# Performance work log

Measured on AMD Instinct MI355X. Metric: run time of the kernel, lower is better.

## Reference

```python
import jax, jax.numpy as jnp
import numpy as np


def setup_inputs() -> dict:
    key = jax.random.key(0)
    ks = jax.random.split(key, 9)
    B, C, H, W = 16, 64, 64, 64
    s = 0.02
    return {
        "x": jax.random.normal(ks[0], (B, C, H, W), dtype=jnp.float32),
        "qw": jax.random.normal(ks[1], (C, C), dtype=jnp.float32) * s,
        "qb": jax.random.normal(ks[2], (C,), dtype=jnp.float32) * s,
        "kw": jax.random.normal(ks[3], (C, C), dtype=jnp.float32) * s,
        "kb": jax.random.normal(ks[4], (C,), dtype=jnp.float32) * s,
        "vw": jax.random.normal(ks[5], (C, C), dtype=jnp.float32) * s,
        "vb": jax.random.normal(ks[6], (C,), dtype=jnp.float32) * s,
        "ow": jax.random.normal(ks[7], (C, C), dtype=jnp.float32) * s,
        "ob": jax.random.normal(ks[8], (C,), dtype=jnp.float32) * s,
    }


def reference(x, qw, qb, kw, kb, vw, vb, ow, ob):
    # x: [B, C, H, W]; 1x1 convs == per-pixel linear maps with weight [out_ch, in_ch]
    B, C, H, W = x.shape
    S = H * W
    xt = x.reshape(B, C, S).transpose(0, 2, 1)  # [B, S, C] tokens over spatial positions
    Q = jnp.einsum("bsc,oc->bso", xt, qw) + qb
    K = jnp.einsum("bsc,oc->bso", xt, kw) + kb
    V = jnp.einsum("bsc,oc->bso", xt, vw) + vb
    scale = 1.0 / jnp.sqrt(jnp.asarray(C, dtype=x.dtype))
    scores = jnp.einsum("bqc,bkc->bqk", Q, K) * scale  # [B, S, S]
    attn = jax.nn.softmax(scores, axis=-1)
    out = jnp.einsum("bqk,bkc->bqc", attn, V)  # [B, S, C]
    out = jnp.einsum("bsc,oc->bso", out, ow) + ob  # out 1x1 conv
    return out.transpose(0, 2, 1).reshape(B, C, H, W)
```

## Files before the change

### kernel.cpp

```cpp
#include <hip/hip_runtime.h>
#include <stdint.h>

#define SS 4096
#define CC 64
#define BB 16

typedef unsigned short u16;
typedef __attribute__((ext_vector_type(8))) __bf16 bf16x8;
typedef __attribute__((ext_vector_type(8))) short short8;
typedef __attribute__((ext_vector_type(4))) float f32x4;

__device__ __forceinline__ uint32_t pkbf(float a, float b) {
    uint32_t ua = __float_as_uint(a) + 0x8000u;
    uint32_t ub = __float_as_uint(b) + 0x8000u;
    return __builtin_amdgcn_perm(ub, ua, 0x07060302u);
}

__global__ void wpre_kernel(const float* __restrict__ qw, const float* __restrict__ kw,
                            const float* __restrict__ vw, const float* __restrict__ ow,
                            u16* __restrict__ wsb)
{
    int idx = blockIdx.x * 256 + threadIdx.x;
    const float* src = (idx < 2048) ? qw : (idx < 4096) ? kw
                     : (idx < 6144) ? vw : ow;
    int pair = idx & 2047;
    ((uint32_t*)wsb)[idx] = pkbf(src[pair * 2], src[pair * 2 + 1]);
}

__global__ __launch_bounds__(256, 4) void qkv_kernel(
    const float* __restrict__ x, const u16* __restrict__ wsb,
    const float* __restrict__ qb, const float* __restrict__ kb,
    const float* __restrict__ vb,
    u16* __restrict__ Q, u16* __restrict__ K, u16* __restrict__ VT)
{
    const int b    = blockIdx.x & 15;
    const int s0   = (blockIdx.x >> 4) << 6;
    const int tid  = threadIdx.x;
    const int w    = tid >> 6;
    const int lane = tid & 63;
    const int lq   = lane & 15;
    const int quad = lane >> 4;

    __shared__ u16 xt[64 * 72];
    __shared__ u16 bounce[4][16 * 72];

    {
        const int sl = tid & 63;
        const int g  = tid >> 6;
        const float* xp = x + (size_t)b * CC * SS + s0 + sl;
#pragma unroll
        for (int i = 0; i < 8; ++i) {
            int p = g + (i << 2);
            float f0 = xp[(size_t)(2 * p) * SS];
            float f1 = xp[(size_t)(2 * p + 1) * SS];
            ((uint32_t*)&xt[sl * 72])[p] = pkbf(f0, f1);
        }
    }
    __syncthreads();

    bf16x8 a0 = *(const bf16x8*)&xt[(w * 16 + lq) * 72 + quad * 8];
    bf16x8 a1 = *(const bf16x8*)&xt[(w * 16 + lq) * 72 + 32 + quad * 8];

    const float QSCALE = 0.125f * 1.44269504088896340736f;

    for (int m = 0; m < 3; ++m) {
        const float* bsrc = (m == 0) ? qb : ((m == 1) ? kb : vb);
        const u16* wm = wsb + m * 4096;
        bf16x8 bfr[2][4];
#pragma unroll
        for (int kc = 0; kc < 2; ++kc)
#pragma unroll
            for (int nt = 0; nt < 4; ++nt)
                bfr[kc][nt] = *(const bf16x8*)&wm[(nt * 16 + lq) * 64 + kc * 32 + quad * 8];

        f32x4 acc[4];
#pragma unroll
        for (int nt = 0; nt < 4; ++nt) {
            float bv = bsrc[nt * 16 + lq];
            acc[nt] = (f32x4){bv, bv, bv, bv};
        }
#pragma unroll
        for (int nt = 0; nt < 4; ++nt) {
            acc[nt] = __builtin_amdgcn_mfma_f32_16x16x32_bf16(a0, bfr[0][nt], acc[nt], 0, 0, 0);
            acc[nt] = __builtin_amdgcn_mfma_f32_16x16x32_bf16(a1, bfr[1][nt], acc[nt], 0, 0, 0);
        }

        if (m == 2) {
#pragma unroll
            for (int nt = 0; nt < 4; ++nt) {
                int c = nt * 16 + lq;
                uint2 pv;
                pv.x = pkbf(acc[nt][0], acc[nt][1]);
                pv.y = pkbf(acc[nt][2], acc[nt][3]);
                *(uint2*)(VT + ((size_t)(b * CC + c)) * SS + s0 + w * 16 + quad * 4) = pv;
            }
        } else {
            const float scl = (m == 0) ? QSCALE : 1.0f;
            u16* bb = bounce[w];
#pragma unroll
            for (int nt = 0; nt < 4; ++nt)
#pragma unroll
                for (int r = 0; r < 4; ++r)
                    bb[(quad * 4 + r) * 72 + nt * 16 + lq] =
                        (u16)((__float_as_uint(acc[nt][r] * scl) + 0x8000u) >> 16);

            const int row = lane >> 2;
            const int ch  = (lane & 3) << 4;
            short8 v0 = *(const short8*)&bb[row * 72 + ch];
            short8 v1 = *(const short8*)&bb[row * 72 + ch + 8];
            u16* dst = ((m == 0) ? Q : K) + ((size_t)(b * SS + s0 + w * 16 + row)) * CC + ch;
            *(short8*)dst = v0;
            *(short8*)(dst + 8) = v1;
        }
    }
}

__global__ __launch_bounds__(256, 2) void flash_kernel(
    const u16* __restrict__ Q, const u16* __restrict__ K,
    const u16* __restrict__ Vt, const u16* __restrict__ owb,
    const float* __restrict__ ob, float* __restrict__ out)
{
    const int b    = blockIdx.x & 15;
    const int q0   = (blockIdx.x >> 4) << 7;
    const int tid  = threadIdx.x;
    const int w    = tid >> 6;
    const int lane = tid & 63;
    const int lq   = lane & 15;
    const int quad = lane >> 4;

    __shared__ u16 lds_k[2][64 * 64];
    __shared__ u16 lds_v[2][64 * 64];
    __shared__ u16 lds_p[8][16 * 72];

    bf16x8 qf[2][2];
#pragma unroll
    for (int g = 0; g < 2; ++g) {
        const u16* qp = Q + ((size_t)(b * SS + q0 + g * 64 + w * 16 + lq)) * CC + quad * 8;
        qf[g][0] = *(const bf16x8*)(qp);
        qf[g][1] = *(const bf16x8*)(qp + 32);
    }

    f32x4 ot[2][4];
#pragma unroll
    for (int g = 0; g < 2; ++g)
#pragma unroll
        for (int ct = 0; ct < 4; ++ct) ot[g][ct] = (f32x4){0.f, 0.f, 0.f, 0.f};
    float lp[2][4] = {{0.f, 0.f, 0.f, 0.f}, {0.f, 0.f, 0.f, 0.f}};

    const int srow = tid >> 2;
    const int a    = tid & 3;
    const u16* kg = K + ((size_t)(b * SS + srow)) * CC + a * 16;
    const u16* vg = Vt + ((size_t)(b * CC + srow)) * SS + a * 16;
    const int sw0 = srow * 64 + (((a << 1)    ) ^ (srow & 7)) * 8;
    const int sw1 = srow * 64 + (((a << 1) | 1) ^ (srow & 7)) * 8;

    {
        short8 k0 = *(const short8*)(kg);
        short8 k1 = *(const short8*)(kg + 8);
        short8 v0 = *(const short8*)(vg);
        short8 v1 = *(const short8*)(vg + 8);
        *(short8*)&lds_k[0][sw0] = k0;
        *(short8*)&lds_k[0][sw1] = k1;
        *(short8*)&lds_v[0][sw0] = v0;
        *(short8*)&lds_v[0][sw1] = v1;
    }

    const int lsw = lq & 7;
    u16* pw0 = lds_p[(w << 1)];
    u16* pw1 = lds_p[(w << 1) | 1];

    for (int kt = 0; kt < 64; ++kt) {
        __syncthreads();
        const int buf = kt & 1;

        const int ktn = (kt + 1) & 63;
        const u16* kgn = kg + (size_t)ktn * (64 * CC);
        const u16* vgn = vg + ktn * 64;
        short8 nk0 = *(const short8*)(kgn);
        short8 nk1 = *(const short8*)(kgn + 8);
        short8 nv0 = *(const short8*)(vgn);
        short8 nv1 = *(const short8*)(vgn + 8);

        bf16x8 kf[2][4];
#pragma unroll
        for (int kc = 0; kc < 2; ++kc)
#pragma unroll
            for (int mt = 0; mt < 4; ++mt)
                kf[kc][mt] = *(const bf16x8*)
                    &lds_k[buf][(mt * 16 + lq) * 64 + (((kc << 2) + quad) ^ lsw) * 8];

        f32x4 sa[2][4];
#pragma unroll
        for (int g = 0; g < 2; ++g)
#pragma unroll
            for (int mt = 0; mt < 4; ++mt) sa[g][mt] = (f32x4){0.f, 0.f, 0.f, 0.f};
#pragma unroll
        for (int g = 0; g < 2; ++g)
#pragma unroll
            for (int kc = 0; kc < 2; ++kc)
#pragma unroll
                for (int mt = 0; mt < 4; ++mt)
                    sa[g][mt] = __builtin_amdgcn_mfma_f32_16x16x32_bf16(
                        kf[kc][mt], qf[g][kc], sa[g][mt], 0, 0, 0);

#pragma unroll
        for (int g = 0; g < 2; ++g) {
            u16* pw = g ? pw1 : pw0;
#pragma unroll
            for (int mt = 0; mt < 4; ++mt) {
                float p0 = __builtin_amdgcn_exp2f(sa[g][mt][0]);
                float p1 = __builtin_amdgcn_exp2f(sa[g][mt][1]);
                float p2 = __builtin_amdgcn_exp2f(sa[g][mt][2]);
                float p3 = __builtin_amdgcn_exp2f(sa[g][mt][3]);
                lp[g][0] += p0; lp[g][1] += p1; lp[g][2] += p2; lp[g][3] += p3;
                uint2 pv;
                pv.x = pkbf(p0, p1);
                pv.y = pkbf(p2, p3);
                *(uint2*)&pw[lq * 72 + mt * 16 + quad * 4] = pv;
            }
        }

        bf16x8 vf[2][4];
#pragma unroll
        for (int kc = 0; kc < 2; ++kc)
#pragma unroll
            for (int ct = 0; ct < 4; ++ct)
                vf[kc][ct] = *(const bf16x8*)
                    &lds_v[buf][(ct * 16 + lq) * 64 + (((kc << 2) + quad) ^ lsw) * 8];

#pragma unroll
        for (int g = 0; g < 2; ++g) {
            const u16* pw = g ? pw1 : pw0;
#pragma unroll
            for (int kc = 0; kc < 2; ++kc) {
                bf16x8 pf = *(const bf16x8*)&pw[lq * 72 + kc * 32 + quad * 8];
#pragma unroll
                for (int ct = 0; ct < 4; ++ct)
                    ot[g][ct] = __builtin_amdgcn_mfma_f32_16x16x32_bf16(
                        vf[kc][ct], pf, ot[g][ct], 0, 0, 0);
            }
        }

        u16* lkd = lds_k[buf ^ 1];
        u16* lvd = lds_v[buf ^ 1];
        *(short8*)&lkd[sw0] = nk0;
        *(short8*)&lkd[sw1] = nk1;
        *(short8*)&lvd[sw0] = nv0;
        *(short8*)&lvd[sw1] = nv1;
    }

    bf16x8 wf[2][4];
#pragma unroll
    for (int kc = 0; kc < 2; ++kc)
#pragma unroll
        for (int nt = 0; nt < 4; ++nt)
            wf[kc][nt] = *(const bf16x8*)&owb[(nt * 16 + lq) * 64 + kc * 32 + quad * 8];
    float bias[4];
#pragma unroll
    for (int nt = 0; nt < 4; ++nt) bias[nt] = ob[nt * 16 + lq];

#pragma unroll
    for (int g = 0; g < 2; ++g) {
        float l = (lp[g][0] + lp[g][1]) + (lp[g][2] + lp[g][3]);
        l += __shfl_xor(l, 16);
        l += __shfl_xor(l, 32);
        const float inv = 1.0f / l;

        u16* po = g ? pw1 : pw0;
#pragma unroll
        for (int ct = 0; ct < 4; ++ct) {
            uint2 pv;
            pv.x = pkbf(ot[g][ct][0] * inv, ot[g][ct][1] * inv);
            pv.y = pkbf(ot[g][ct][2] * inv, ot[g][ct][3] * inv);
            *(uint2*)&po[lq * 72 + ct * 16 + quad * 4] = pv;
        }
        bf16x8 oa0 = *(const bf16x8*)&po[lq * 72 + quad * 8];
        bf16x8 oa1 = *(const bf16x8*)&po[lq * 72 + 32 + quad * 8];

        f32x4 acc[4];
#pragma unroll
        for (int nt = 0; nt < 4; ++nt)
            acc[nt] = (f32x4){bias[nt], bias[nt], bias[nt], bias[nt]};
#pragma unroll
        for (int nt = 0; nt < 4; ++nt) {
            acc[nt] = __builtin_amdgcn_mfma_f32_16x16x32_bf16(oa0, wf[0][nt], acc[nt], 0, 0, 0);
            acc[nt] = __builtin_amdgcn_mfma_f32_16x16x32_bf16(oa1, wf[1][nt], acc[nt], 0, 0, 0);
        }
#pragma unroll
        for (int nt = 0; nt < 4; ++nt) {
            float* dst = out + ((size_t)(b * CC + nt * 16 + lq)) * SS
                       + q0 + g * 64 + w * 16 + quad * 4;
            *(f32x4*)dst = acc[nt];
        }
    }
}

extern "C" void kernel_launch(void* const* d_in, const int* in_sizes, int n_in,
                              void* d_out, int out_size, void* d_ws, size_t ws_size,
                              hipStream_t stream)
{
    const float* x  = (const float*)d_in[0];
    const float* qw = (const float*)d_in[1];
    const float* qb = (const float*)d_in[2];
    const float* kw = (const float*)d_in[3];
    const float* kb = (const float*)d_in[4];
    const float* vw = (const float*)d_in[5];
    const float* vb = (const float*)d_in[6];
    const float* ow = (const float*)d_in[7];
    const float* ob = (const float*)d_in[8];
    float* out = (float*)d_out;

    const size_t T = (size_t)BB * SS * CC;
    u16* WSB = (u16*)d_ws;
    u16* Q   = WSB + 4 * 4096;
    u16* K   = Q + T;
    u16* VT  = K + T;

    wpre_kernel<<<dim3(32), dim3(256), 0, stream>>>(qw, kw, vw, ow, WSB);
    qkv_kernel<<<dim3(BB * 64), dim3(256), 0, stream>>>(x, WSB, qb, kb, vb, Q, K, VT);
    flash_kernel<<<dim3(BB * 32), dim3(256), 0, stream>>>(Q, K, VT, WSB + 3 * 4096, ob, out);
}
```

Before: 188.9 us.

## Split flash kernel key tiles across waves and load QKV inputs directly to registers

The flash kernel now splits each 64-key tile between wave pairs. Each wave covers 64 queries but only 32 keys, so it loads half the K fragments and a reduced V fragment set from LDS per query group. The two key-halves' partial outputs and row sums are then merged through LDS before the output projection, which only half the waves perform. The QKV kernel drops its LDS transpose of x and reads the strided fp32 values straight into MFMA operand registers. This cuts LDS traffic per MFMA, at the cost of more accumulator registers, a final cross-wave reduction, and less-coalesced global reads of x.

```diff
diff --git a/kernel.cpp b/kernel.cpp
--- a/kernel.cpp
+++ b/kernel.cpp
@@ -41,25 +41,23 @@
     const int lq   = lane & 15;
     const int quad = lane >> 4;
 
-    __shared__ u16 xt[64 * 72];
     __shared__ u16 bounce[4][16 * 72];
 
-    {
-        const int sl = tid & 63;
-        const int g  = tid >> 6;
-        const float* xp = x + (size_t)b * CC * SS + s0 + sl;
-#pragma unroll
-        for (int i = 0; i < 8; ++i) {
-            int p = g + (i << 2);
-            float f0 = xp[(size_t)(2 * p) * SS];
-            float f1 = xp[(size_t)(2 * p + 1) * SS];
-            ((uint32_t*)&xt[sl * 72])[p] = pkbf(f0, f1);
-        }
-    }
-    __syncthreads();
-
-    bf16x8 a0 = *(const bf16x8*)&xt[(w * 16 + lq) * 72 + quad * 8];
-    bf16x8 a1 = *(const bf16x8*)&xt[(w * 16 + lq) * 72 + 32 + quad * 8];
+    const int sm = s0 + w * 16 + lq;
+    const float* xp = x + (size_t)b * CC * SS + sm;
+    float xf[16];
+#pragma unroll
+    for (int kc = 0; kc < 2; ++kc)
+#pragma unroll
+        for (int j = 0; j < 8; ++j)
+            xf[kc * 8 + j] = xp[(size_t)(kc * 32 + quad * 8 + j) * SS];
+
+    union { uint32_t u[4]; bf16x8 v; } A0, A1;
+#pragma unroll
+    for (int p = 0; p < 4; ++p) {
+        A0.u[p] = pkbf(xf[2 * p],     xf[2 * p + 1]);
+        A1.u[p] = pkbf(xf[8 + 2 * p], xf[8 + 2 * p + 1]);
+    }
 
     const float QSCALE = 0.125f * 1.44269504088896340736f;
 
@@ -81,8 +79,8 @@
         }
 #pragma unroll
         for (int nt = 0; nt < 4; ++nt) {
-            acc[nt] = __builtin_amdgcn_mfma_f32_16x16x32_bf16(a0, bfr[0][nt], acc[nt], 0, 0, 0);
-            acc[nt] = __builtin_amdgcn_mfma_f32_16x16x32_bf16(a1, bfr[1][nt], acc[nt], 0, 0, 0);
+            acc[nt] = __builtin_amdgcn_mfma_f32_16x16x32_bf16(A0.v, bfr[0][nt], acc[nt], 0, 0, 0);
+            acc[nt] = __builtin_amdgcn_mfma_f32_16x16x32_bf16(A1.v, bfr[1][nt], acc[nt], 0, 0, 0);
         }
 
         if (m == 2) {
@@ -124,28 +122,29 @@
     const int q0   = (blockIdx.x >> 4) << 7;
     const int tid  = threadIdx.x;
     const int w    = tid >> 6;
+    const int qh   = w & 1;
+    const int kh   = w >> 1;
     const int lane = tid & 63;
     const int lq   = lane & 15;
     const int quad = lane >> 4;
 
-    __shared__ u16 lds_k[2][64 * 64];
-    __shared__ u16 lds_v[2][64 * 64];
-    __shared__ u16 lds_p[8][16 * 72];
-
-    bf16x8 qf[2][2];
-#pragma unroll
-    for (int g = 0; g < 2; ++g) {
-        const u16* qp = Q + ((size_t)(b * SS + q0 + g * 64 + w * 16 + lq)) * CC + quad * 8;
+    __shared__ u16 lds_s[2][8192];
+    __shared__ u16 lds_p[4][2048];
+
+    bf16x8 qf[4][2];
+#pragma unroll
+    for (int g = 0; g < 4; ++g) {
+        const u16* qp = Q + ((size_t)(b * SS + q0 + qh * 64 + g * 16 + lq)) * CC + quad * 8;
         qf[g][0] = *(const bf16x8*)(qp);
         qf[g][1] = *(const bf16x8*)(qp + 32);
     }
 
-    f32x4 ot[2][4];
-#pragma unroll
-    for (int g = 0; g < 2; ++g)
+    f32x4 ot[4][4];
+#pragma unroll
+    for (int g = 0; g < 4; ++g)
 #pragma unroll
         for (int ct = 0; ct < 4; ++ct) ot[g][ct] = (f32x4){0.f, 0.f, 0.f, 0.f};
-    float lp[2][4] = {{0.f, 0.f, 0.f, 0.f}, {0.f, 0.f, 0.f, 0.f}};
+    float lp[4] = {0.f, 0.f, 0.f, 0.f};
 
     const int srow = tid >> 2;
     const int a    = tid & 3;
@@ -159,15 +158,15 @@
         short8 k1 = *(const short8*)(kg + 8);
         short8 v0 = *(const short8*)(vg);
         short8 v1 = *(const short8*)(vg + 8);
-        *(short8*)&lds_k[0][sw0] = k0;
-        *(short8*)&lds_k[0][sw1] = k1;
-        *(short8*)&lds_v[0][sw0] = v0;
-        *(short8*)&lds_v[0][sw1] = v1;
+        *(short8*)&lds_s[0][sw0] = k0;
+        *(short8*)&lds_s[0][sw1] = k1;
+        *(short8*)&lds_s[0][4096 + sw0] = v0;
+        *(short8*)&lds_s[0][4096 + sw1] = v1;
     }
 
     const int lsw = lq & 7;
-    u16* pw0 = lds_p[(w << 1)];
-    u16* pw1 = lds_p[(w << 1) | 1];
+    u16* pw = lds_p[w];
+    const int ps = lq & 1;
 
     for (int kt = 0; kt < 64; ++kt) {
         __syncthreads();
@@ -181,116 +180,128 @@
         short8 nv0 = *(const short8*)(vgn);
         short8 nv1 = *(const short8*)(vgn + 8);
 
-        bf16x8 kf[2][4];
+        bf16x8 kf[2][2];
 #pragma unroll
         for (int kc = 0; kc < 2; ++kc)
 #pragma unroll
-            for (int mt = 0; mt < 4; ++mt)
+            for (int mt = 0; mt < 2; ++mt)
                 kf[kc][mt] = *(const bf16x8*)
-                    &lds_k[buf][(mt * 16 + lq) * 64 + (((kc << 2) + quad) ^ lsw) * 8];
-
-        f32x4 sa[2][4];
-#pragma unroll
-        for (int g = 0; g < 2; ++g)
-#pragma unroll
-            for (int mt = 0; mt < 4; ++mt) sa[g][mt] = (f32x4){0.f, 0.f, 0.f, 0.f};
-#pragma unroll
-        for (int g = 0; g < 2; ++g)
+                    &lds_s[buf][(kh * 32 + mt * 16 + lq) * 64 + (((kc << 2) + quad) ^ lsw) * 8];
+
+        bf16x8 vf[4];
+#pragma unroll
+        for (int ct = 0; ct < 4; ++ct)
+            vf[ct] = *(const bf16x8*)
+                &lds_s[buf][4096 + (ct * 16 + lq) * 64 + (((kh << 2) + quad) ^ lsw) * 8];
+
+#pragma unroll
+        for (int g = 0; g < 4; ++g) {
+            f32x4 sa[2];
+            sa[0] = (f32x4){0.f, 0.f, 0.f, 0.f};
+            sa[1] = (f32x4){0.f, 0.f, 0.f, 0.f};
 #pragma unroll
             for (int kc = 0; kc < 2; ++kc)
 #pragma unroll
-                for (int mt = 0; mt < 4; ++mt)
-                    sa[g][mt] = __builtin_amdgcn_mfma_f32_16x16x32_bf16(
-                        kf[kc][mt], qf[g][kc], sa[g][mt], 0, 0, 0);
-
-#pragma unroll
-        for (int g = 0; g < 2; ++g) {
-            u16* pw = g ? pw1 : pw0;
-#pragma unroll
-            for (int mt = 0; mt < 4; ++mt) {
-                float p0 = __builtin_amdgcn_exp2f(sa[g][mt][0]);
-                float p1 = __builtin_amdgcn_exp2f(sa[g][mt][1]);
-                float p2 = __builtin_amdgcn_exp2f(sa[g][mt][2]);
-                float p3 = __builtin_amdgcn_exp2f(sa[g][mt][3]);
-                lp[g][0] += p0; lp[g][1] += p1; lp[g][2] += p2; lp[g][3] += p3;
+                for (int mt = 0; mt < 2; ++mt)
+                    sa[mt] = __builtin_amdgcn_mfma_f32_16x16x32_bf16(
+                        kf[kc][mt], qf[g][kc], sa[mt], 0, 0, 0);
+
+            const int pr = (g * 16 + lq) * 32;
+#pragma unroll
+            for (int mt = 0; mt < 2; ++mt) {
+                float p0 = __builtin_amdgcn_exp2f(sa[mt][0]);
+                float p1 = __builtin_amdgcn_exp2f(sa[mt][1]);
+                float p2 = __builtin_amdgcn_exp2f(sa[mt][2]);
+                float p3 = __builtin_amdgcn_exp2f(sa[mt][3]);
+                lp[g] += (p0 + p1) + (p2 + p3);
                 uint2 pv;
                 pv.x = pkbf(p0, p1);
                 pv.y = pkbf(p2, p3);
-                *(uint2*)&pw[lq * 72 + mt * 16 + quad * 4] = pv;
-            }
-        }
-
-        bf16x8 vf[2][4];
+                *(uint2*)&pw[pr + ((mt ^ ps) << 4) + quad * 4] = pv;
+            }
+        }
+
+#pragma unroll
+        for (int g = 0; g < 4; ++g) {
+            const int pr = (g * 16 + lq) * 32;
+            bf16x8 pf = *(const bf16x8*)&pw[pr + (((quad >> 1) ^ ps) << 4) + (quad & 1) * 8];
+#pragma unroll
+            for (int ct = 0; ct < 4; ++ct)
+                ot[g][ct] = __builtin_amdgcn_mfma_f32_16x16x32_bf16(
+                    vf[ct], pf, ot[g][ct], 0, 0, 0);
+        }
+
+        u16* ld = lds_s[buf ^ 1];
+        *(short8*)&ld[sw0] = nk0;
+        *(short8*)&ld[sw1] = nk1;
+        *(short8*)&ld[4096 + sw0] = nv0;
+        *(short8*)&ld[4096 + sw1] = nv1;
+    }
+
+#pragma unroll
+    for (int g = 0; g < 4; ++g) {
+        lp[g] += __shfl_xor(lp[g], 16);
+        lp[g] += __shfl_xor(lp[g], 32);
+    }
+
+    float* mb  = (float*)&lds_s[0][0];
+    float* lpb = (float*)&lds_p[2][0];
+
+    __syncthreads();
+    if (kh == 1) {
+#pragma unroll
+        for (int g = 0; g < 4; ++g) {
+#pragma unroll
+            for (int ct = 0; ct < 4; ++ct)
+                *(f32x4*)&mb[qh * 4096 + (g * 16 + lq) * 64 + ct * 16 + quad * 4] = ot[g][ct];
+            if (quad == 0) lpb[qh * 64 + g * 16 + lq] = lp[g];
+        }
+    }
+    __syncthreads();
+
+    if (kh == 0) {
+        bf16x8 wf[2][4];
 #pragma unroll
         for (int kc = 0; kc < 2; ++kc)
 #pragma unroll
-            for (int ct = 0; ct < 4; ++ct)
-                vf[kc][ct] = *(const bf16x8*)
-                    &lds_v[buf][(ct * 16 + lq) * 64 + (((kc << 2) + quad) ^ lsw) * 8];
-
-#pragma unroll
-        for (int g = 0; g < 2; ++g) {
-            const u16* pw = g ? pw1 : pw0;
-#pragma unroll
-            for (int kc = 0; kc < 2; ++kc) {
-                bf16x8 pf = *(const bf16x8*)&pw[lq * 72 + kc * 32 + quad * 8];
-#pragma unroll
-                for (int ct = 0; ct < 4; ++ct)
-                    ot[g][ct] = __builtin_amdgcn_mfma_f32_16x16x32_bf16(
-                        vf[kc][ct], pf, ot[g][ct], 0, 0, 0);
-            }
-        }
-
-        u16* lkd = lds_k[buf ^ 1];
-        u16* lvd = lds_v[buf ^ 1];
-        *(short8*)&lkd[sw0] = nk0;
-        *(short8*)&lkd[sw1] = nk1;
-        *(short8*)&lvd[sw0] = nv0;
-        *(short8*)&lvd[sw1] = nv1;
-    }
-
-    bf16x8 wf[2][4];
-#pragma unroll
-    for (int kc = 0; kc < 2; ++kc)
-#pragma unroll
-        for (int nt = 0; nt < 4; ++nt)
-            wf[kc][nt] = *(const bf16x8*)&owb[(nt * 16 + lq) * 64 + kc * 32 + quad * 8];
-    float bias[4];
-#pragma unroll
-    for (int nt = 0; nt < 4; ++nt) bias[nt] = ob[nt * 16 + lq];
-
-#pragma unroll
-    for (int g = 0; g < 2; ++g) {
-        float l = (lp[g][0] + lp[g][1]) + (lp[g][2] + lp[g][3]);
-        l += __shfl_xor(l, 16);
-        l += __shfl_xor(l, 32);
-        const float inv = 1.0f / l;
-
-        u16* po = g ? pw1 : pw0;
-#pragma unroll
-        for (int ct = 0; ct < 4; ++ct) {
-            uint2 pv;
-            pv.x = pkbf(ot[g][ct][0] * inv, ot[g][ct][1] * inv);
-            pv.y = pkbf(ot[g][ct][2] * inv, ot[g][ct][3] * inv);
-            *(uint2*)&po[lq * 72 + ct * 16 + quad * 4] = pv;
-        }
-        bf16x8 oa0 = *(const bf16x8*)&po[lq * 72 + quad * 8];
-        bf16x8 oa1 = *(const bf16x8*)&po[lq * 72 + 32 + quad * 8];
-
-        f32x4 acc[4];
-#pragma unroll
-        for (int nt = 0; nt < 4; ++nt)
-            acc[nt] = (f32x4){bias[nt], bias[nt], bias[nt], bias[nt]};
-#pragma unroll
-        for (int nt = 0; nt < 4; ++nt) {
-            acc[nt] = __builtin_amdgcn_mfma_f32_16x16x32_bf16(oa0, wf[0][nt], acc[nt], 0, 0, 0);
-            acc[nt] = __builtin_amdgcn_mfma_f32_16x16x32_bf16(oa1, wf[1][nt], acc[nt], 0, 0, 0);
-        }
-#pragma unroll
-        for (int nt = 0; nt < 4; ++nt) {
-            float* dst = out + ((size_t)(b * CC + nt * 16 + lq)) * SS
-                       + q0 + g * 64 + w * 16 + quad * 4;
-            *(f32x4*)dst = acc[nt];
+            for (int nt = 0; nt < 4; ++nt)
+                wf[kc][nt] = *(const bf16x8*)&owb[(nt * 16 + lq) * 64 + kc * 32 + quad * 8];
+        float bias[4];
+#pragma unroll
+        for (int nt = 0; nt < 4; ++nt) bias[nt] = ob[nt * 16 + lq];
+
+        u16* po = lds_p[w];
+#pragma unroll
+        for (int g = 0; g < 4; ++g) {
+            const float l = lp[g] + lpb[qh * 64 + g * 16 + lq];
+            const float inv = 1.0f / l;
+
+#pragma unroll
+            for (int ct = 0; ct < 4; ++ct) {
+                f32x4 o2 = *(const f32x4*)&mb[qh * 4096 + (g * 16 + lq) * 64 + ct * 16 + quad * 4];
+                uint2 pv;
+                pv.x = pkbf((ot[g][ct][0] + o2[0]) * inv, (ot[g][ct][1] + o2[1]) * inv);
+                pv.y = pkbf((ot[g][ct][2] + o2[2]) * inv, (ot[g][ct][3] + o2[3]) * inv);
+                *(uint2*)&po[lq * 72 + ct * 16 + quad * 4] = pv;
+            }
+            bf16x8 oa0 = *(const bf16x8*)&po[lq * 72 + quad * 8];
+            bf16x8 oa1 = *(const bf16x8*)&po[lq * 72 + 32 + quad * 8];
+
+            f32x4 acc[4];
+#pragma unroll
+            for (int nt = 0; nt < 4; ++nt)
+                acc[nt] = (f32x4){bias[nt], bias[nt], bias[nt], bias[nt]};
+#pragma unroll
+            for (int nt = 0; nt < 4; ++nt) {
+                acc[nt] = __builtin_amdgcn_mfma_f32_16x16x32_bf16(oa0, wf[0][nt], acc[nt], 0, 0, 0);
+                acc[nt] = __builtin_amdgcn_mfma_f32_16x16x32_bf16(oa1, wf[1][nt], acc[nt], 0, 0, 0);
+            }
+#pragma unroll
+            for (int nt = 0; nt < 4; ++nt) {
+                float* dst = out + ((size_t)(b * CC + nt * 16 + lq)) * SS
+                           + q0 + qh * 64 + g * 16 + quad * 4;
+                *(f32x4*)dst = acc[nt];
+            }
         }
     }
 }
```

Result: slower. 216.5 us (+14.6%).

## Load V fragments directly from global and drop LDS staging for x and V

Applied to the files above, without the earlier changes.

In the flash kernel, V^T tiles are no longer staged through double-buffered LDS. Each lane now loads its MFMA operand fragments straight from global memory at the top of every key tile. In the QKV kernel, x is read per lane into registers and packed to bf16 without the shared transpose buffer or its barrier. This trims LDS footprint and traffic, which may allow more blocks per CU. The cost is global loads on the critical path of each iteration with no prefetch ahead of use, plus strided, less coalesced x reads.

```diff
diff --git a/kernel.cpp b/kernel.cpp
--- a/kernel.cpp
+++ b/kernel.cpp
@@ -41,25 +41,23 @@
     const int lq   = lane & 15;
     const int quad = lane >> 4;
 
-    __shared__ u16 xt[64 * 72];
     __shared__ u16 bounce[4][16 * 72];
 
-    {
-        const int sl = tid & 63;
-        const int g  = tid >> 6;
-        const float* xp = x + (size_t)b * CC * SS + s0 + sl;
-#pragma unroll
-        for (int i = 0; i < 8; ++i) {
-            int p = g + (i << 2);
-            float f0 = xp[(size_t)(2 * p) * SS];
-            float f1 = xp[(size_t)(2 * p + 1) * SS];
-            ((uint32_t*)&xt[sl * 72])[p] = pkbf(f0, f1);
-        }
-    }
-    __syncthreads();
-
-    bf16x8 a0 = *(const bf16x8*)&xt[(w * 16 + lq) * 72 + quad * 8];
-    bf16x8 a1 = *(const bf16x8*)&xt[(w * 16 + lq) * 72 + 32 + quad * 8];
+    const int sm = s0 + w * 16 + lq;
+    const float* xp = x + (size_t)b * CC * SS + sm;
+    float xf[16];
+#pragma unroll
+    for (int kc = 0; kc < 2; ++kc)
+#pragma unroll
+        for (int j = 0; j < 8; ++j)
+            xf[kc * 8 + j] = xp[(size_t)(kc * 32 + quad * 8 + j) * SS];
+
+    union { uint32_t u[4]; bf16x8 v; } A0, A1;
+#pragma unroll
+    for (int p = 0; p < 4; ++p) {
+        A0.u[p] = pkbf(xf[2 * p],     xf[2 * p + 1]);
+        A1.u[p] = pkbf(xf[8 + 2 * p], xf[8 + 2 * p + 1]);
+    }
 
     const float QSCALE = 0.125f * 1.44269504088896340736f;
 
@@ -81,8 +79,8 @@
         }
 #pragma unroll
         for (int nt = 0; nt < 4; ++nt) {
-            acc[nt] = __builtin_amdgcn_mfma_f32_16x16x32_bf16(a0, bfr[0][nt], acc[nt], 0, 0, 0);
-            acc[nt] = __builtin_amdgcn_mfma_f32_16x16x32_bf16(a1, bfr[1][nt], acc[nt], 0, 0, 0);
+            acc[nt] = __builtin_amdgcn_mfma_f32_16x16x32_bf16(A0.v, bfr[0][nt], acc[nt], 0, 0, 0);
+            acc[nt] = __builtin_amdgcn_mfma_f32_16x16x32_bf16(A1.v, bfr[1][nt], acc[nt], 0, 0, 0);
         }
 
         if (m == 2) {
@@ -129,7 +127,6 @@
     const int quad = lane >> 4;
 
     __shared__ u16 lds_k[2][64 * 64];
-    __shared__ u16 lds_v[2][64 * 64];
     __shared__ u16 lds_p[8][16 * 72];
 
     bf16x8 qf[2][2];
@@ -140,6 +137,11 @@
         qf[g][1] = *(const bf16x8*)(qp + 32);
     }
 
+    const u16* vp[4];
+#pragma unroll
+    for (int ct = 0; ct < 4; ++ct)
+        vp[ct] = Vt + ((size_t)(b * CC + ct * 16 + lq)) * SS + quad * 8;
+
     f32x4 ot[2][4];
 #pragma unroll
     for (int g = 0; g < 2; ++g)
@@ -150,19 +152,14 @@
     const int srow = tid >> 2;
     const int a    = tid & 3;
     const u16* kg = K + ((size_t)(b * SS + srow)) * CC + a * 16;
-    const u16* vg = Vt + ((size_t)(b * CC + srow)) * SS + a * 16;
     const int sw0 = srow * 64 + (((a << 1)    ) ^ (srow & 7)) * 8;
     const int sw1 = srow * 64 + (((a << 1) | 1) ^ (srow & 7)) * 8;
 
     {
         short8 k0 = *(const short8*)(kg);
         short8 k1 = *(const short8*)(kg + 8);
-        short8 v0 = *(const short8*)(vg);
-        short8 v1 = *(const short8*)(vg + 8);
         *(short8*)&lds_k[0][sw0] = k0;
         *(short8*)&lds_k[0][sw1] = k1;
-        *(short8*)&lds_v[0][sw0] = v0;
-        *(short8*)&lds_v[0][sw1] = v1;
     }
 
     const int lsw = lq & 7;
@@ -173,13 +170,17 @@
         __syncthreads();
         const int buf = kt & 1;
 
+        bf16x8 vfr[2][4];
+#pragma unroll
+        for (int kc = 0; kc < 2; ++kc)
+#pragma unroll
+            for (int ct = 0; ct < 4; ++ct)
+                vfr[kc][ct] = *(const bf16x8*)(vp[ct] + kc * 32);
+
         const int ktn = (kt + 1) & 63;
         const u16* kgn = kg + (size_t)ktn * (64 * CC);
-        const u16* vgn = vg + ktn * 64;
         short8 nk0 = *(const short8*)(kgn);
         short8 nk1 = *(const short8*)(kgn + 8);
-        short8 nv0 = *(const short8*)(vgn);
-        short8 nv1 = *(const short8*)(vgn + 8);
 
         bf16x8 kf[2][4];
 #pragma unroll
@@ -220,14 +221,6 @@
             }
         }
 
-        bf16x8 vf[2][4];
-#pragma unroll
-        for (int kc = 0; kc < 2; ++kc)
-#pragma unroll
-            for (int ct = 0; ct < 4; ++ct)
-                vf[kc][ct] = *(const bf16x8*)
-                    &lds_v[buf][(ct * 16 + lq) * 64 + (((kc << 2) + quad) ^ lsw) * 8];
-
 #pragma unroll
         for (int g = 0; g < 2; ++g) {
             const u16* pw = g ? pw1 : pw0;
@@ -237,16 +230,15 @@
 #pragma unroll
                 for (int ct = 0; ct < 4; ++ct)
                     ot[g][ct] = __builtin_amdgcn_mfma_f32_16x16x32_bf16(
-                        vf[kc][ct], pf, ot[g][ct], 0, 0, 0);
+                        vfr[kc][ct], pf, ot[g][ct], 0, 0, 0);
             }
         }
 
+#pragma unroll
+        for (int ct = 0; ct < 4; ++ct) vp[ct] += 64;
         u16* lkd = lds_k[buf ^ 1];
-        u16* lvd = lds_v[buf ^ 1];
         *(short8*)&lkd[sw0] = nk0;
         *(short8*)&lkd[sw1] = nk1;
-        *(short8*)&lvd[sw0] = nv0;
-        *(short8*)&lvd[sw1] = nv1;
     }
 
     bf16x8 wf[2][4];
```

New measurement: 262.2 us. 1.39x slower.

## Fold weight bf16 conversion into consumers and swizzle P tile in LDS

Applied to the files above, without the earlier changes.

Removes the separate weight-prepack kernel. The QKV kernel now converts Q/K/V weights to bf16 into shared memory itself and reuses the x tile as its bounce buffer. The flash kernel converts the output-projection weights from fp32 directly. The P/O staging buffer in the flash kernel changes from padded 72-wide rows to 64-wide rows with an XOR swizzle to avoid bank conflicts and save LDS. This saves a kernel launch, but every QKV block now redundantly converts all three weight matrices.

```diff
diff --git a/kernel.cpp b/kernel.cpp
--- a/kernel.cpp
+++ b/kernel.cpp
@@ -16,21 +16,22 @@
     return __builtin_amdgcn_perm(ub, ua, 0x07060302u);
 }
 
-__global__ void wpre_kernel(const float* __restrict__ qw, const float* __restrict__ kw,
-                            const float* __restrict__ vw, const float* __restrict__ ow,
-                            u16* __restrict__ wsb)
-{
-    int idx = blockIdx.x * 256 + threadIdx.x;
-    const float* src = (idx < 2048) ? qw : (idx < 4096) ? kw
-                     : (idx < 6144) ? vw : ow;
-    int pair = idx & 2047;
-    ((uint32_t*)wsb)[idx] = pkbf(src[pair * 2], src[pair * 2 + 1]);
+__device__ __forceinline__ bf16x8 ldw8(const float* p) {
+    f32x4 lo = *(const f32x4*)(p);
+    f32x4 hi = *(const f32x4*)(p + 4);
+    union { uint32_t u[4]; bf16x8 v; } r;
+    r.u[0] = pkbf(lo[0], lo[1]);
+    r.u[1] = pkbf(lo[2], lo[3]);
+    r.u[2] = pkbf(hi[0], hi[1]);
+    r.u[3] = pkbf(hi[2], hi[3]);
+    return r.v;
 }
 
 __global__ __launch_bounds__(256, 4) void qkv_kernel(
-    const float* __restrict__ x, const u16* __restrict__ wsb,
-    const float* __restrict__ qb, const float* __restrict__ kb,
-    const float* __restrict__ vb,
+    const float* __restrict__ x,
+    const float* __restrict__ qw, const float* __restrict__ qb,
+    const float* __restrict__ kw, const float* __restrict__ kb,
+    const float* __restrict__ vw, const float* __restrict__ vb,
     u16* __restrict__ Q, u16* __restrict__ K, u16* __restrict__ VT)
 {
     const int b    = blockIdx.x & 15;
@@ -41,9 +42,20 @@
     const int lq   = lane & 15;
     const int quad = lane >> 4;
 
+    __shared__ u16 wt[3][64 * 72];
     __shared__ u16 xt[64 * 72];
-    __shared__ u16 bounce[4][16 * 72];
-
+
+    for (int m = 0; m < 3; ++m) {
+        const float* wsrc = (m == 0) ? qw : ((m == 1) ? kw : vw);
+#pragma unroll
+        for (int i = 0; i < 8; ++i) {
+            int p  = tid + (i << 8);
+            int o  = p >> 5;
+            int cp = p & 31;
+            const float* wp = wsrc + o * 64 + cp * 2;
+            ((uint32_t*)&wt[m][o * 72])[cp] = pkbf(wp[0], wp[1]);
+        }
+    }
     {
         const int sl = tid & 63;
         const int g  = tid >> 6;
@@ -60,18 +72,20 @@
 
     bf16x8 a0 = *(const bf16x8*)&xt[(w * 16 + lq) * 72 + quad * 8];
     bf16x8 a1 = *(const bf16x8*)&xt[(w * 16 + lq) * 72 + 32 + quad * 8];
+    __syncthreads();
+
+    u16* bb = xt + w * (16 * 72);
 
     const float QSCALE = 0.125f * 1.44269504088896340736f;
 
     for (int m = 0; m < 3; ++m) {
         const float* bsrc = (m == 0) ? qb : ((m == 1) ? kb : vb);
-        const u16* wm = wsb + m * 4096;
         bf16x8 bfr[2][4];
 #pragma unroll
         for (int kc = 0; kc < 2; ++kc)
 #pragma unroll
             for (int nt = 0; nt < 4; ++nt)
-                bfr[kc][nt] = *(const bf16x8*)&wm[(nt * 16 + lq) * 64 + kc * 32 + quad * 8];
+                bfr[kc][nt] = *(const bf16x8*)&wt[m][(nt * 16 + lq) * 72 + kc * 32 + quad * 8];
 
         f32x4 acc[4];
 #pragma unroll
@@ -96,7 +110,6 @@
             }
         } else {
             const float scl = (m == 0) ? QSCALE : 1.0f;
-            u16* bb = bounce[w];
 #pragma unroll
             for (int nt = 0; nt < 4; ++nt)
 #pragma unroll
@@ -117,7 +130,7 @@
 
 __global__ __launch_bounds__(256, 2) void flash_kernel(
     const u16* __restrict__ Q, const u16* __restrict__ K,
-    const u16* __restrict__ Vt, const u16* __restrict__ owb,
+    const u16* __restrict__ Vt, const float* __restrict__ ow,
     const float* __restrict__ ob, float* __restrict__ out)
 {
     const int b    = blockIdx.x & 15;
@@ -130,7 +143,7 @@
 
     __shared__ u16 lds_k[2][64 * 64];
     __shared__ u16 lds_v[2][64 * 64];
-    __shared__ u16 lds_p[8][16 * 72];
+    __shared__ u16 lds_p[8][16 * 64];
 
     bf16x8 qf[2][2];
 #pragma unroll
@@ -216,7 +229,7 @@
                 uint2 pv;
                 pv.x = pkbf(p0, p1);
                 pv.y = pkbf(p2, p3);
-                *(uint2*)&pw[lq * 72 + mt * 16 + quad * 4] = pv;
+                *(uint2*)&pw[lq * 64 + (((mt * 2 + (quad >> 1)) ^ lsw) << 3) + (quad & 1) * 4] = pv;
             }
         }
 
@@ -233,7 +246,8 @@
             const u16* pw = g ? pw1 : pw0;
 #pragma unroll
             for (int kc = 0; kc < 2; ++kc) {
-                bf16x8 pf = *(const bf16x8*)&pw[lq * 72 + kc * 32 + quad * 8];
+                bf16x8 pf = *(const bf16x8*)
+                    &pw[lq * 64 + (((kc * 4 + quad) ^ lsw) << 3)];
 #pragma unroll
                 for (int ct = 0; ct < 4; ++ct)
                     ot[g][ct] = __builtin_amdgcn_mfma_f32_16x16x32_bf16(
@@ -254,7 +268,7 @@
     for (int kc = 0; kc < 2; ++kc)
 #pragma unroll
         for (int nt = 0; nt < 4; ++nt)
-            wf[kc][nt] = *(const bf16x8*)&owb[(nt * 16 + lq) * 64 + kc * 32 + quad * 8];
+            wf[kc][nt] = ldw8(ow + (nt * 16 + lq) * 64 + kc * 32 + quad * 8);
     float bias[4];
 #pragma unroll
     for (int nt = 0; nt < 4; ++nt) bias[nt] = ob[nt * 16 + lq];
@@ -272,10 +286,10 @@
             uint2 pv;
             pv.x = pkbf(ot[g][ct][0] * inv, ot[g][ct][1] * inv);
             pv.y = pkbf(ot[g][ct][2] * inv, ot[g][ct][3] * inv);
-            *(uint2*)&po[lq * 72 + ct * 16 + quad * 4] = pv;
-        }
-        bf16x8 oa0 = *(const bf16x8*)&po[lq * 72 + quad * 8];
-        bf16x8 oa1 = *(const bf16x8*)&po[lq * 72 + 32 + quad * 8];
+            *(uint2*)&po[lq * 64 + (((ct * 2 + (quad >> 1)) ^ lsw) << 3) + (quad & 1) * 4] = pv;
+        }
+        bf16x8 oa0 = *(const bf16x8*)&po[lq * 64 + (((0 * 4 + quad) ^ lsw) << 3)];
+        bf16x8 oa1 = *(const bf16x8*)&po[lq * 64 + (((1 * 4 + quad) ^ lsw) << 3)];
 
         f32x4 acc[4];
 #pragma unroll
@@ -311,12 +325,10 @@
     float* out = (float*)d_out;
 
     const size_t T = (size_t)BB * SS * CC;
-    u16* WSB = (u16*)d_ws;
-    u16* Q   = WSB + 4 * 4096;
-    u16* K   = Q + T;
-    u16* VT  = K + T;
-
-    wpre_kernel<<<dim3(32), dim3(256), 0, stream>>>(qw, kw, vw, ow, WSB);
-    qkv_kernel<<<dim3(BB * 64), dim3(256), 0, stream>>>(x, WSB, qb, kb, vb, Q, K, VT);
-    flash_kernel<<<dim3(BB * 32), dim3(256), 0, stream>>>(Q, K, VT, WSB + 3 * 4096, ob, out);
-}
+    u16* Q  = (u16*)d_ws;
+    u16* K  = Q + T;
+    u16* VT = K + T;
+
+    qkv_kernel<<<dim3(BB * 64), dim3(256), 0, stream>>>(x, qw, qb, kw, kb, vw, vb, Q, K, VT);
+    flash_kernel<<<dim3(BB * 32), dim3(256), 0, stream>>>(Q, K, VT, ow, ob, out);
+}
```

Result: faster. 183.1 us (-3.1%).
